# Performance work log

Hardware: AMD Instinct MI355X
Metric: run time of the kernel (lower is better)

Reference implementation:

```python
import jax, jax.numpy as jnp
import numpy as np

B, T, D, H = 16, 2048, 1024, 1024  # batch, seq (effective block_size), n_embed, head_size


def setup_inputs() -> dict:
    key = jax.random.key(0)
    k1, k2, k3, k4 = jax.random.split(key, 4)
    x = jax.random.normal(k1, (B, T, D), dtype=jnp.float32)
    # torch Linear weight is [out,in]; store as [in,out] for x @ W
    s = 1.0 / np.sqrt(D)
    Wq = jax.random.uniform(k2, (D, H), dtype=jnp.float32, minval=-s, maxval=s)
    Wk = jax.random.uniform(k3, (D, H), dtype=jnp.float32, minval=-s, maxval=s)
    Wv = jax.random.uniform(k4, (D, H), dtype=jnp.float32, minval=-s, maxval=s)
    return {"x": x, "Wq": Wq, "Wk": Wk, "Wv": Wv}


def reference(x, Wq, Wk, Wv):
    # Single-head causal self-attention, NO 1/sqrt(d) scaling (faithful to source).
    q = x @ Wq  # [B,T,H]
    k = x @ Wk  # [B,T,H]
    v = x @ Wv  # [B,T,H]
    w = jnp.einsum('bth,bsh->bts', q, k)  # [B,T,T]
    Tn = x.shape[1]
    causal = jnp.tril(jnp.ones((Tn, Tn), dtype=bool))
    w = jnp.where(causal, w, -jnp.inf)
    w = jax.nn.softmax(w, axis=-1)
    # dropout is identity in eval mode
    out = jnp.einsum('bts,bsh->bth', w, v)  # [B,T,H]
    return out
```

## Files before the change

kernel.cpp:

```cpp
#include <hip/hip_runtime.h>
#include <hip/hip_bf16.h>


typedef _Float16 half8 __attribute__((ext_vector_type(8)));
typedef _Float16 half4v __attribute__((ext_vector_type(4)));
typedef float floatx4 __attribute__((ext_vector_type(4)));

#define TB 16
#define TT 2048
#define TD 1024

#define BARRIER() asm volatile("s_barrier" ::: "memory")

__global__ void cvt_f32_f16(const float* __restrict__ in, _Float16* __restrict__ out, long n) {
    long i = ((long)blockIdx.x * blockDim.x + threadIdx.x) * 4;
    long stride = (long)gridDim.x * blockDim.x * 4;
    for (; i < n; i += stride) {
        float4 f = *(const float4*)(in + i);
        half4v h;
        h[0] = (_Float16)f.x; h[1] = (_Float16)f.y;
        h[2] = (_Float16)f.z; h[3] = (_Float16)f.w;
        *(half4v*)(out + i) = h;
    }
}

__global__ void transpose_cvt_w(const float* __restrict__ in, _Float16* __restrict__ out) {
    __shared__ float tile[32][33];
    const int bx = blockIdx.x * 32, by = blockIdx.y * 32;
    const int tx = threadIdx.x, ty = threadIdx.y;
#pragma unroll
    for (int i = ty; i < 32; i += 8) tile[i][tx] = in[(long)(by + i) * 1024 + bx + tx];
    __syncthreads();
#pragma unroll
    for (int i = ty; i < 32; i += 8) out[(long)(bx + i) * 1024 + by + tx] = (_Float16)tile[tx][i];
}

__device__ __forceinline__ void gload16(const _Float16* g, _Float16* l) {
    __builtin_amdgcn_global_load_lds((const __attribute__((address_space(1))) void*)g,
                                     (__attribute__((address_space(3))) void*)l, 16, 0, 0);
}

template <int MODE>
__global__ __launch_bounds__(512, 2) void gemm256(const _Float16* __restrict__ A,
                                                  const _Float16* __restrict__ B,
                                                  void* __restrict__ Cout,
                                                  void* __restrict__ Cout2,
                                                  int K, int lda, int ldb, int ldc,
                                                  long sAb, long sBb, long sCb,
                                                  int tilesN, int tilesM, int nb) {
    __shared__ _Float16 lds[32768];
    const int tid = threadIdx.x, lane = tid & 63, w = tid >> 6;
    const int wr = w >> 2, wc = w & 3;

    int b, ti, tj;
    if (MODE == 2) {
        const int grp = nb * 4;
        const int g = blockIdx.x / grp;
        ti = tilesM - 1 - g;
        int i2 = blockIdx.x - g * grp;
        const int q = grp >> 3, r = grp & 7, xcd = i2 & 7, idx = i2 >> 3;
        i2 = (xcd < r ? xcd * (q + 1) : r * (q + 1) + (xcd - r) * q) + idx;
        b = i2 >> 2; tj = i2 & 3;
    } else {
        int bx = blockIdx.x;
        const int nwg = gridDim.x, q = nwg >> 3, r = nwg & 7, xcd = bx & 7, idx = bx >> 3;
        bx = (xcd < r ? xcd * (q + 1) : r * (q + 1) + (xcd - r) * q) + idx;
        b = blockIdx.y;
        if (MODE == 1) {
            int rd = bx; ti = 0;
            while (rd > ti) { rd -= ti + 1; ++ti; }
            tj = rd;
        } else {
            ti = bx / tilesN; tj = bx % tilesN;
        }
    }
    A += (long)b * sAb;
    B += (long)b * sBb;
    const long m0 = (long)ti * 256, n0 = (long)tj * 256;
    const int nkt = (MODE == 2) ? (ti + 1) * 4 : (K >> 6);

    const int row0 = tid >> 2;
    const int co   = (((tid & 3) ^ ((tid >> 3) & 3)) << 3);
    const int fcol = ((((lane >> 4) ^ (lane >> 1)) & 3) << 3);
    const int arow = wr * 128 + (lane & 15);
    const int brow = wc * 64 + (lane & 15);

    auto Abase = [&](int buf, int kk) { return lds + ((buf * 2 + kk) << 13); };

    auto stageA = [&](int buf, int kk, int kt) {
        const long kb = (long)kt * 64 + kk * 32 + co;
        _Float16* d = Abase(buf, kk) + (w << 9);
        gload16(A + (m0 + row0) * (long)lda + kb, d);
        gload16(A + (m0 + row0 + 128) * (long)lda + kb, d + 4096);
    };
    auto ldA = [&](int buf, int kk, int m) {
        return *(const half8*)(Abase(buf, kk) + (arow + m * 16) * 32 + fcol);
    };
    const _Float16* Bg = B + (long)(n0 + brow) * ldb + ((lane >> 4) << 3);
    auto gatherB = [&](half8* bf, int kt, int kk) {
#pragma unroll
        for (int nn = 0; nn < 4; ++nn)
            bf[nn] = *(const half8*)(Bg + (long)nn * 16 * ldb + kt * 64 + kk * 32);
    };

    floatx4 acc[8][4] = {};
    half8 afE[4], afO[4], bfE[4], bfO[4];

#define MFMA_Q(MH, BF, AF)                                                             \
    __builtin_amdgcn_s_setprio(1);                                                     \
    _Pragma("unroll") for (int mm = 0; mm < 4; ++mm)                                   \
    _Pragma("unroll") for (int nn = 0; nn < 4; ++nn)                                   \
        acc[(MH)*4 + mm][nn] =                                                         \
            __builtin_amdgcn_mfma_f32_16x16x32_f16(AF[mm], BF[nn], acc[(MH)*4 + mm][nn], 0, 0, 0); \
    __builtin_amdgcn_s_setprio(0);

    {
        const int k1 = (1 < nkt) ? 1 : 0;
        stageA(0, 0, 0); stageA(0, 1, 0); stageA(1, 0, k1);
        gatherB(bfE, 0, 0);
    }
    asm volatile("s_waitcnt vmcnt(2)" ::: "memory");
    BARRIER();
#pragma unroll
    for (int mm = 0; mm < 4; ++mm) afE[mm] = ldA(0, 0, mm);

    for (int t = 0; t < nkt; ++t) {
        const int cur = t & 1, nxt = cur ^ 1;
        const int kt1 = (t + 1 < nkt) ? t + 1 : nkt - 1;
        const int kt2 = (t + 2 < nkt) ? t + 2 : nkt - 1;
        MFMA_Q(0, bfE, afE)
#pragma unroll
        for (int mm = 0; mm < 4; ++mm) afO[mm] = ldA(cur, 0, mm + 4);
        gatherB(bfO, t, 1);
        stageA(nxt, 1, kt1);
        asm volatile("s_waitcnt vmcnt(12)" ::: "memory");
        BARRIER();
        MFMA_Q(1, bfE, afO)
#pragma unroll
        for (int mm = 0; mm < 4; ++mm) afE[mm] = ldA(cur, 1, mm);
        BARRIER();
        MFMA_Q(0, bfO, afE)
#pragma unroll
        for (int mm = 0; mm < 4; ++mm) afO[mm] = ldA(cur, 1, mm + 4);
        gatherB(bfE, kt1, 0);
        stageA(cur, 0, kt2);
        asm volatile("s_waitcnt vmcnt(12)" ::: "memory");
        BARRIER();
        MFMA_Q(1, bfO, afO)
#pragma unroll
        for (int mm = 0; mm < 4; ++mm) afE[mm] = ldA(nxt, 0, mm);
        BARRIER();
    }
#undef MFMA_Q
    asm volatile("s_waitcnt vmcnt(0) lgkmcnt(0)" ::: "memory");

    const int r4 = (lane >> 4) * 4, ccol = lane & 15;
    if (MODE != 2) {
        _Float16* C;
        long nb0 = n0;
        if (MODE == 3 && n0 >= TD) { C = (_Float16*)Cout2; nb0 = n0 - TD; }
        else                        C = (_Float16*)Cout + (long)b * sCb;
#pragma unroll
        for (int m = 0; m < 8; ++m) {
            const long rbase = m0 + wr * 128 + m * 16 + r4;
#pragma unroll
            for (int n = 0; n < 4; ++n) {
                const long cbase = nb0 + wc * 64 + n * 16 + ccol;
#pragma unroll
                for (int j = 0; j < 4; ++j)
                    C[(rbase + j) * (long)ldc + cbase] = (_Float16)acc[m][n][j];
            }
        }
    } else {
        float* C = (float*)Cout + (long)b * sCb;
#pragma unroll
        for (int m = 0; m < 8; ++m) {
            const long rbase = m0 + wr * 128 + m * 16 + r4;
#pragma unroll
            for (int n = 0; n < 4; ++n) {
                const long cbase = n0 + wc * 64 + n * 16 + ccol;
#pragma unroll
                for (int j = 0; j < 4; ++j)
                    C[(rbase + j) * (long)ldc + cbase] = acc[m][n][j];
            }
        }
    }
}

__global__ __launch_bounds__(256) void softmax_rows_f16(_Float16* __restrict__ S, int T) {
    const int wv = threadIdx.x >> 6, lane = threadIdx.x & 63;
    const long row = (long)blockIdx.x * 4 + wv;
    const int t = (int)(row & (T - 1));
    _Float16* s = S + row * (long)T;
    const int nstore = ((t >> 8) + 1) << 8;

    float v[4][8];
    float mx = -__builtin_inff();
#pragma unroll
    for (int c = 0; c < 4; ++c) {
        const int col0 = (c * 64 + lane) * 8;
        if (col0 <= t) {
            half8 hv = *(const half8*)(s + col0);
#pragma unroll
            for (int j = 0; j < 8; ++j) {
                v[c][j] = (col0 + j <= t) ? (float)hv[j] : -__builtin_inff();
                mx = fmaxf(mx, v[c][j]);
            }
        } else {
#pragma unroll
            for (int j = 0; j < 8; ++j) v[c][j] = -__builtin_inff();
        }
    }
#pragma unroll
    for (int o = 32; o; o >>= 1) mx = fmaxf(mx, __shfl_xor(mx, o));

    float sum = 0.f;
#pragma unroll
    for (int c = 0; c < 4; ++c)
#pragma unroll
        for (int j = 0; j < 8; ++j) {
            float p = __expf(v[c][j] - mx);
            v[c][j] = p;
            sum += p;
        }
#pragma unroll
    for (int o = 32; o; o >>= 1) sum += __shfl_xor(sum, o);
    const float inv = 1.f / sum;

#pragma unroll
    for (int c = 0; c < 4; ++c) {
        const int col0 = (c * 64 + lane) * 8;
        if (col0 < nstore) {
            half8 o;
#pragma unroll
            for (int j = 0; j < 8; ++j) o[j] = (_Float16)(v[c][j] * inv);
            *(half8*)(s + col0) = o;
        }
    }
}

extern "C" void kernel_launch(void* const* d_in, const int* in_sizes, int n_in,
                              void* d_out, int out_size, void* d_ws, size_t ws_size,
                              hipStream_t stream) {
    const float* x  = (const float*)d_in[0];
    const float* Wq = (const float*)d_in[1];
    const float* Wk = (const float*)d_in[2];
    const float* Wv = (const float*)d_in[3];
    float* out = (float*)d_out;

    const size_t XB = (size_t)TB * TT * TD;

    _Float16* x16 = (_Float16*)d_out;
    _Float16* Kh  = (_Float16*)d_out + XB;

    char* ws = (char*)d_ws;
    size_t off = 0;
    auto carve = [&](size_t bytes) { char* p = ws + off; off = (off + bytes + 255) & ~(size_t)255; return p; };
    _Float16* wqt = (_Float16*)carve((size_t)TD * TD * 2);
    _Float16* wkt = (_Float16*)carve((size_t)TD * TD * 2);
    _Float16* wvt = (_Float16*)carve((size_t)TD * TD * 2);
    _Float16* Qh  = (_Float16*)carve(XB * 2);
    _Float16* Vt  = (_Float16*)carve(XB * 2);

    const size_t CH = (size_t)TT * TT * 2;
    int NB = 16;
    while (NB > 1 && off + (size_t)NB * CH > ws_size) NB >>= 1;
    _Float16* Sc = (_Float16*)carve((size_t)NB * CH);

    cvt_f32_f16<<<2048, 256, 0, stream>>>(x, x16, (long)XB);
    transpose_cvt_w<<<dim3(32, 32), dim3(32, 8), 0, stream>>>(Wq, wqt);
    transpose_cvt_w<<<dim3(32, 32), dim3(32, 8), 0, stream>>>(Wk, wkt);
    transpose_cvt_w<<<dim3(32, 32), dim3(32, 8), 0, stream>>>(Wv, wvt);

    gemm256<3><<<dim3(128 * 8, 1), 512, 0, stream>>>(x16, wqt, Qh, Kh, TD, TD, TD, TD,
                                                     0, 0, 0, 8, 128, 0);
    gemm256<0><<<dim3(4 * 8, TB), 512, 0, stream>>>(wvt, x16, Vt, nullptr, TD, TD, TD, TT,
                                                    0, (long)TT * TD, (long)TD * TT, 8, 4, 0);

    for (int cb = 0; cb < TB; cb += NB) {
        gemm256<1><<<dim3(36, NB), 512, 0, stream>>>(Qh + (size_t)cb * TT * TD,
                                                     Kh + (size_t)cb * TT * TD, Sc, nullptr,
                                                     TD, TD, TD, TT,
                                                     (long)TT * TD, (long)TT * TD, (long)TT * TT, 8, 8, 0);
        softmax_rows_f16<<<NB * TT / 4, 256, 0, stream>>>(Sc, TT);
        gemm256<2><<<dim3(NB * 32, 1), 512, 0, stream>>>(Sc, Vt + (size_t)cb * TD * TT,
                                                         out + (size_t)cb * TT * TD, nullptr, TT,
                                                         TT, TT, TD,
                                                         (long)TT * TT, (long)TD * TT, (long)TT * TD, 4, 8, NB);
    }
}
```

Baseline: 578.2 us.

## Stage B through LDS with a triple-buffered 32-wide K pipeline

Restructures the GEMM main loop so that both A and B tiles are staged into LDS through async global-to-LDS loads. It replaces the previous setup, where A went through LDS with double buffering and B was gathered straight from global memory into registers. The K step shrinks to 32 with a three-buffer ring, leaving one barrier per iteration and two stages in flight. The aim is to cut the uncoalesced direct global B loads and the number of barriers, at the cost of more LDS use (96 KB per block), which may lower occupancy with launch bounds of 2 blocks per CU.

```diff
diff --git a/kernel.cpp b/kernel.cpp
--- a/kernel.cpp
+++ b/kernel.cpp
@@ -48,7 +48,7 @@
                                                   int K, int lda, int ldb, int ldc,
                                                   long sAb, long sBb, long sCb,
                                                   int tilesN, int tilesM, int nb) {
-    __shared__ _Float16 lds[32768];
+    __shared__ _Float16 lds[49152];
     const int tid = threadIdx.x, lane = tid & 63, w = tid >> 6;
     const int wr = w >> 2, wc = w & 3;
 
@@ -77,7 +77,7 @@
     A += (long)b * sAb;
     B += (long)b * sBb;
     const long m0 = (long)ti * 256, n0 = (long)tj * 256;
-    const int nkt = (MODE == 2) ? (ti + 1) * 4 : (K >> 6);
+    const int nkt = (MODE == 2) ? (ti + 1) * 8 : (K >> 5);
 
     const int row0 = tid >> 2;
     const int co   = (((tid & 3) ^ ((tid >> 3) & 3)) << 3);
@@ -85,73 +85,64 @@
     const int arow = wr * 128 + (lane & 15);
     const int brow = wc * 64 + (lane & 15);
 
-    auto Abase = [&](int buf, int kk) { return lds + ((buf * 2 + kk) << 13); };
-
-    auto stageA = [&](int buf, int kk, int kt) {
-        const long kb = (long)kt * 64 + kk * 32 + co;
-        _Float16* d = Abase(buf, kk) + (w << 9);
+    auto Abase = [&](int buf) { return lds + (buf << 13); };
+    auto Bbase = [&](int buf) { return lds + 24576 + (buf << 13); };
+
+    auto stageA = [&](int buf, int kt) {
+        const long kb = (long)kt * 32 + co;
+        _Float16* d = Abase(buf) + (w << 9);
         gload16(A + (m0 + row0) * (long)lda + kb, d);
         gload16(A + (m0 + row0 + 128) * (long)lda + kb, d + 4096);
     };
-    auto ldA = [&](int buf, int kk, int m) {
-        return *(const half8*)(Abase(buf, kk) + (arow + m * 16) * 32 + fcol);
-    };
-    const _Float16* Bg = B + (long)(n0 + brow) * ldb + ((lane >> 4) << 3);
-    auto gatherB = [&](half8* bf, int kt, int kk) {
-#pragma unroll
-        for (int nn = 0; nn < 4; ++nn)
-            bf[nn] = *(const half8*)(Bg + (long)nn * 16 * ldb + kt * 64 + kk * 32);
+    auto stageB = [&](int buf, int kt) {
+        const long kb = (long)kt * 32 + co;
+        _Float16* d = Bbase(buf) + (w << 9);
+        gload16(B + (n0 + row0) * (long)ldb + kb, d);
+        gload16(B + (n0 + row0 + 128) * (long)ldb + kb, d + 4096);
+    };
+    auto ldA = [&](int buf, int m) {
+        return *(const half8*)(Abase(buf) + (arow + m * 16) * 32 + fcol);
+    };
+    auto ldB = [&](int buf, int n) {
+        return *(const half8*)(Bbase(buf) + (brow + n * 16) * 32 + fcol);
     };
 
     floatx4 acc[8][4] = {};
-    half8 afE[4], afO[4], bfE[4], bfO[4];
-
-#define MFMA_Q(MH, BF, AF)                                                             \
-    __builtin_amdgcn_s_setprio(1);                                                     \
-    _Pragma("unroll") for (int mm = 0; mm < 4; ++mm)                                   \
-    _Pragma("unroll") for (int nn = 0; nn < 4; ++nn)                                   \
-        acc[(MH)*4 + mm][nn] =                                                         \
-            __builtin_amdgcn_mfma_f32_16x16x32_f16(AF[mm], BF[nn], acc[(MH)*4 + mm][nn], 0, 0, 0); \
-    __builtin_amdgcn_s_setprio(0);
+    half8 af[8], bf[4];
 
     {
         const int k1 = (1 < nkt) ? 1 : 0;
-        stageA(0, 0, 0); stageA(0, 1, 0); stageA(1, 0, k1);
-        gatherB(bfE, 0, 0);
-    }
-    asm volatile("s_waitcnt vmcnt(2)" ::: "memory");
+        stageA(0, 0); stageB(0, 0);
+        stageA(1, k1); stageB(1, k1);
+    }
+    asm volatile("s_waitcnt vmcnt(4)" ::: "memory");
     BARRIER();
-#pragma unroll
-    for (int mm = 0; mm < 4; ++mm) afE[mm] = ldA(0, 0, mm);
-
+
+    int cur = 0;
     for (int t = 0; t < nkt; ++t) {
-        const int cur = t & 1, nxt = cur ^ 1;
-        const int kt1 = (t + 1 < nkt) ? t + 1 : nkt - 1;
+        const int b2 = (cur + 2 >= 3) ? cur - 1 : cur + 2;
         const int kt2 = (t + 2 < nkt) ? t + 2 : nkt - 1;
-        MFMA_Q(0, bfE, afE)
-#pragma unroll
-        for (int mm = 0; mm < 4; ++mm) afO[mm] = ldA(cur, 0, mm + 4);
-        gatherB(bfO, t, 1);
-        stageA(nxt, 1, kt1);
-        asm volatile("s_waitcnt vmcnt(12)" ::: "memory");
+#pragma unroll
+        for (int nn = 0; nn < 4; ++nn) bf[nn] = ldB(cur, nn);
+#pragma unroll
+        for (int mm = 0; mm < 8; ++mm) af[mm] = ldA(cur, mm);
+        stageA(b2, kt2); stageB(b2, kt2);
+        __builtin_amdgcn_s_setprio(1);
+#pragma unroll
+        for (int mm = 0; mm < 4; ++mm)
+#pragma unroll
+            for (int nn = 0; nn < 4; ++nn)
+                acc[mm][nn] = __builtin_amdgcn_mfma_f32_16x16x32_f16(af[mm], bf[nn], acc[mm][nn], 0, 0, 0);
+#pragma unroll
+        for (int mm = 4; mm < 8; ++mm)
+#pragma unroll
+            for (int nn = 0; nn < 4; ++nn)
+                acc[mm][nn] = __builtin_amdgcn_mfma_f32_16x16x32_f16(af[mm], bf[nn], acc[mm][nn], 0, 0, 0);
+        __builtin_amdgcn_s_setprio(0);
+        asm volatile("s_waitcnt vmcnt(4)" ::: "memory");
         BARRIER();
-        MFMA_Q(1, bfE, afO)
-#pragma unroll
-        for (int mm = 0; mm < 4; ++mm) afE[mm] = ldA(cur, 1, mm);
-        BARRIER();
-        MFMA_Q(0, bfO, afE)
-#pragma unroll
-        for (int mm = 0; mm < 4; ++mm) afO[mm] = ldA(cur, 1, mm + 4);
-        gatherB(bfE, kt1, 0);
-        stageA(cur, 0, kt2);
-        asm volatile("s_waitcnt vmcnt(12)" ::: "memory");
-        BARRIER();
-        MFMA_Q(1, bfO, afO)
-#pragma unroll
-        for (int mm = 0; mm < 4; ++mm) afE[mm] = ldA(nxt, 0, mm);
-        BARRIER();
-    }
-#undef MFMA_Q
+        cur = (cur + 1 >= 3) ? 0 : cur + 1;
+    }
     asm volatile("s_waitcnt vmcnt(0) lgkmcnt(0)" ::: "memory");
 
     const int r4 = (lane >> 4) * 4, ccol = lane & 15;
```

Result: faster. 485.2 us (-16.1%).
